# Performance work log

Measured on AMD Instinct MI355X. Metric: run time of the kernel, lower is better.

## Reference

```python
import jax, jax.numpy as jnp
from jax import lax
import numpy as np

B, COND_C = 16, 256
IN_C, OUT_C, K = 64, 64, 3
H = W = 128
N_PARAM = K * K * IN_C * OUT_C + OUT_C  # 36928


def setup_inputs() -> dict:
    key = jax.random.key(0)
    k1, k2, k3, k4 = jax.random.split(key, 4)
    x = jax.random.normal(k1, (B, IN_C, H, W), dtype=jnp.float32)
    conditioning = jax.random.normal(k2, (B, COND_C), dtype=jnp.float32)
    # nn.Linear(cond_c, n_param): weight [n_param, cond_c], bias [n_param]
    W_cond = jax.random.normal(k3, (N_PARAM, COND_C), dtype=jnp.float32) * 0.02
    b_cond = jax.random.normal(k4, (N_PARAM,), dtype=jnp.float32) * 0.02
    return {"x": x, "conditioning": conditioning, "W_cond": W_cond, "b_cond": b_cond}


def reference(x, conditioning, W_cond, b_cond):
    # Hypernetwork: Linear + tanh*5 (ConditionerActivation)
    w_b = jnp.tanh(conditioning @ W_cond.T + b_cond) * 5.0  # [B, N_PARAM]
    bias = w_b[:, -OUT_C:]                                   # [B, out_c]
    w = w_b[:, :-OUT_C].reshape(B, OUT_C, IN_C, K, K)        # per-sample OIHW

    def conv_one(xi, wi, bi):
        # xi: [in_c, H, W], wi: [out_c, in_c, K, K], bi: [out_c]
        y = lax.conv_general_dilated(
            xi[None], wi,
            window_strides=(1, 1),
            padding=[(1, 1), (1, 1)],
            dimension_numbers=("NCHW", "OIHW", "NCHW"),
        )[0]
        return y + bi[:, None, None]

    return jax.vmap(conv_one)(x, w, bias)  # [B, out_c, H, W]
```

## Files before the change

### kernel.cpp

```cpp
#include <hip/hip_runtime.h>
#include <math.h>
#include <stdint.h>

#define B_    16
#define CONDC 256
#define ICn   64
#define OCn   64
#define Hn    128
#define Wn    128
#define NW    36864
#define NPARAM 36928

typedef _Float16 half8 __attribute__((ext_vector_type(8)));
typedef _Float16 half4 __attribute__((ext_vector_type(4)));
typedef float f32x4 __attribute__((ext_vector_type(4)));
typedef float f32x16 __attribute__((ext_vector_type(16)));

__global__ __launch_bounds__(256) void prep(const float* __restrict__ x,
                                            const float* __restrict__ cond,
                                            const float* __restrict__ Wc,
                                            const float* __restrict__ bc,
                                            _Float16* __restrict__ xt,
                                            _Float16* __restrict__ wt,
                                            float* __restrict__ bias) {
    __shared__ float smem[8256];
    const int tid = threadIdx.x;
    int bx = blockIdx.x;

    if (bx < 2080) {
        const int b  = bx / 130;
        const int yp = bx - b * 130;
        _Float16* rowhalf = xt + (size_t)(b * 130 + yp) * (130 * 64);
        if (yp == 0 || yp == 129) {
            half4 z = (half4){0, 0, 0, 0};
            for (int u = tid; u < 2080; u += 256) *(half4*)(rowhalf + u * 4) = z;
            return;
        }
        float* ls = smem;
        for (int i = tid; i < 2048; i += 256) {
            int ic = i >> 5;
            float4 v = ((const float4*)x)[(((size_t)(b * 64 + ic) * 128) + (yp - 1)) * 32 + (i & 31)];
            int xx = (i & 31) * 4;
            float* lr = ls + ic * 129 + xx;
            lr[0] = v.x; lr[1] = v.y; lr[2] = v.z; lr[3] = v.w;
        }
        __syncthreads();
        for (int u2 = tid; u2 < 2080; u2 += 256) {
            int xp = u2 >> 4, ic4 = (u2 & 15) << 2;
            half4 pk;
            if (xp == 0 || xp == 129) pk = (half4){0, 0, 0, 0};
            else {
                pk[0] = (_Float16)ls[(ic4    ) * 129 + xp - 1];
                pk[1] = (_Float16)ls[(ic4 + 1) * 129 + xp - 1];
                pk[2] = (_Float16)ls[(ic4 + 2) * 129 + xp - 1];
                pk[3] = (_Float16)ls[(ic4 + 3) * 129 + xp - 1];
            }
            *(half4*)(rowhalf + u2 * 4) = pk;
        }
    } else {
        const int g = bx - 2080;
        _Float16* cl = (_Float16*)smem;
        for (int i = tid; i < 1024; i += 256) {
            float4 v = ((const float4*)cond)[i];
            half4 pk = { (_Float16)v.x, (_Float16)v.y, (_Float16)v.z, (_Float16)v.w };
            *(half4*)(cl + i * 4) = pk;
        }
        __syncthreads();
        const int w = tid >> 6, l = tid & 63;
        const int n = l & 15, r4 = l >> 4;
        const int pb = g * 64 + w * 16;

        half8 bfr[8];
        #pragma unroll
        for (int kk = 0; kk < 8; ++kk)
            bfr[kk] = *(const half8*)(cl + n * 256 + kk * 32 + r4 * 8);

        f32x4 acc = (f32x4){0.f, 0.f, 0.f, 0.f};
        const float* wr = Wc + (size_t)(pb + n) * 256 + r4 * 8;
        #pragma unroll
        for (int kk = 0; kk < 8; ++kk) {
            float4 u0 = *(const float4*)(wr + kk * 32);
            float4 u1 = *(const float4*)(wr + kk * 32 + 4);
            half8 av;
            av[0] = (_Float16)u0.x; av[1] = (_Float16)u0.y; av[2] = (_Float16)u0.z; av[3] = (_Float16)u0.w;
            av[4] = (_Float16)u1.x; av[5] = (_Float16)u1.y; av[6] = (_Float16)u1.z; av[7] = (_Float16)u1.w;
            acc = __builtin_amdgcn_mfma_f32_16x16x32_f16(av, bfr[kk], acc, 0, 0, 0);
        }
        #pragma unroll
        for (int j = 0; j < 4; ++j) {
            int p = pb + r4 * 4 + j;
            float v = tanhf(acc[j] + bc[p]) * 5.0f;
            if (p < NW) {
                int oc = p / 576, rem = p - oc * 576;
                int ic = rem / 9,  t  = rem - ic * 9;
                int icq = ic >> 4, icl = ic & 15;
                wt[((((size_t)n * 4 + icq) * 9 + t) * 64 + oc) * 16 + icl] = (_Float16)v;
            } else {
                bias[n * 64 + (p - NW)] = v;
            }
        }
    }
}

__global__ __launch_bounds__(512, 2) void conv_v4(const _Float16* __restrict__ xt,
                                                  const _Float16* __restrict__ wt,
                                                  const float* __restrict__ bias,
                                                  float* __restrict__ out) {
    __shared__ _Float16 xs[2][12288];
    const int tid = threadIdx.x;
    const int l   = tid & 63;
    const int w   = tid >> 6;
    const int px  = l & 31;
    const int jj  = l >> 5;
    const int ot  = w & 1;
    const int rg  = w >> 1;
    const int b   = blockIdx.z;
    const int X0  = blockIdx.x * 32;
    const int Y0g = blockIdx.y * 16;

    const _Float16* xbase = xt + ((size_t)(b * 130 + Y0g) * 130 + X0) * 64;
    const _Float16* wbat  = wt + (size_t)b * 36864 + (size_t)(ot * 32 + px) * 16 + jj * 8;

    int offkw[3];
    #pragma unroll
    for (int kw = 0; kw < 3; ++kw) {
        int c = (px + kw) * 2 + jj;
        offkw[kw] = (c ^ ((c >> 3) & 7)) * 16;
    }
    const int Lb = rg * 4;

    #define STAGEQ(ICQ, BUF) do {                                                       \
        _Pragma("unroll")                                                               \
        for (int it = 0; it < 3; ++it) {                                                \
            int d  = it * 512 + tid;                                                    \
            int dc = d < 1296 ? d : 1295;                                               \
            int row = (int)((unsigned)dc / 72u);                                        \
            int c   = dc - row * 72;                                                    \
            int cs  = c ^ ((c >> 3) & 7);                                               \
            const _Float16* src = xbase + (size_t)row * 8320 + (cs >> 1) * 64           \
                                + (ICQ) * 16 + (cs & 1) * 8;                            \
            __builtin_amdgcn_global_load_lds(                                           \
                (const __attribute__((address_space(1))) void*)src,                     \
                (__attribute__((address_space(3))) void*)((__attribute__((address_space(3))) char*)xs + (BUF) * 24576 + (it * 512 + (tid & ~63)) * 16), \
                16, 0, 0);                                                              \
        } } while (0)

    STAGEQ(0, 0);
    half8 A[2][9];
    #pragma unroll
    for (int t = 0; t < 9; ++t) A[0][t] = *(const half8*)(wbat + t * 1024);

    f32x16 acc[4];
    #pragma unroll
    for (int r = 0; r < 4; ++r) acc[r] = (f32x16){};

    #pragma unroll
    for (int icq = 0; icq < 4; ++icq) {
        const int cur = icq & 1;
        if (icq < 3) {
            STAGEQ(icq + 1, cur ^ 1);
            asm volatile("s_waitcnt vmcnt(3)" ::: "memory");
        } else {
            asm volatile("s_waitcnt vmcnt(0)" ::: "memory");
        }
        __builtin_amdgcn_sched_barrier(0);
        __builtin_amdgcn_s_barrier();
        __builtin_amdgcn_sched_barrier(0);

        if (icq < 3) {
            #pragma unroll
            for (int t = 0; t < 9; ++t)
                A[cur ^ 1][t] = *(const half8*)(wbat + ((icq + 1) * 9 + t) * 1024);
        }

        const char* bufb = (const char*)xs + cur * 24576;
        #pragma unroll
        for (int kw = 0; kw < 3; ++kw) {
            half8 Bf[6];
            #pragma unroll
            for (int iy = 0; iy < 6; ++iy)
                Bf[iy] = *(const half8*)(bufb + (Lb + iy) * 1152 + offkw[kw]);
            #pragma unroll
            for (int iy = 0; iy < 6; ++iy) {
                #pragma unroll
                for (int kh = 0; kh < 3; ++kh) {
                    const int r = iy - kh;
                    if (r >= 0 && r < 4)
                        acc[r] = __builtin_amdgcn_mfma_f32_32x32x16_f16(A[cur][kh * 3 + kw], Bf[iy], acc[r], 0, 0, 0);
                }
            }
        }
        asm volatile("s_waitcnt lgkmcnt(0)" ::: "memory");
        __builtin_amdgcn_sched_barrier(0);
        __builtin_amdgcn_s_barrier();
        __builtin_amdgcn_sched_barrier(0);
    }
    #undef STAGEQ

    const float* bb = bias + b * 64;
    #pragma unroll
    for (int r = 0; r < 4; ++r) {
        const int yo = Y0g + Lb + r;
        float* ob = out + (((size_t)(b * 64 + ot * 32)) * 128 + yo) * 128 + X0 + px;
        #pragma unroll
        for (int reg = 0; reg < 16; ++reg) {
            const int ocl = (reg & 3) + 8 * (reg >> 2) + 4 * jj;
            ob[(size_t)ocl * 16384] = acc[r][reg] + bb[ot * 32 + ocl];
        }
    }
}

__global__ __launch_bounds__(256) void cond_gemm(const float* __restrict__ cond,
                                                 const float* __restrict__ Wc,
                                                 const float* __restrict__ bc,
                                                 float* __restrict__ wb) {
    __shared__ float condl[B_][CONDC + 1];
    __shared__ float Wl[16][CONDC + 1];
    const int tid = threadIdx.x;
    const int p0 = blockIdx.x * 16;
    for (int i = tid; i < B_ * CONDC; i += 256) condl[i >> 8][i & 255] = cond[i];
    for (int i = tid; i < 16 * CONDC; i += 256) {
        int pl = i >> 8, k = i & 255;
        Wl[pl][k] = Wc[(p0 + pl) * CONDC + k];
    }
    __syncthreads();
    const int pl = tid >> 4;
    const int b  = tid & 15;
    float acc = bc[p0 + pl];
    #pragma unroll 8
    for (int k = 0; k < CONDC; ++k) acc += Wl[pl][k] * condl[b][k];
    wb[b * NPARAM + p0 + pl] = tanhf(acc) * 5.0f;
}

#define TS  32
#define OG  8
#define ICC 8
__global__ __launch_bounds__(256) void conv_kernel(const float* __restrict__ x,
                                                   const float* __restrict__ wb,
                                                   float* __restrict__ out) {
    __shared__ float fxs[ICC][TS + 2][TS + 2];
    __shared__ float ws[OG][ICC][9];
    const int tid = threadIdx.x;
    const int b   = blockIdx.z;
    const int ocg = blockIdx.y * OG;
    const int tx0 = (blockIdx.x & 3) * TS;
    const int ty0 = (blockIdx.x >> 2) * TS;
    const int px  = (tid & 15) * 2;
    const int py  = (tid >> 4) * 2;
    float acc[OG][4];
    #pragma unroll
    for (int o = 0; o < OG; ++o)
        #pragma unroll
        for (int q = 0; q < 4; ++q) acc[o][q] = 0.0f;
    const float* wbase = wb + b * NPARAM;
    for (int ic0 = 0; ic0 < ICn; ic0 += ICC) {
        for (int i = tid; i < ICC * (TS + 2) * (TS + 2); i += 256) {
            int icl = i / ((TS + 2) * (TS + 2));
            int rem = i % ((TS + 2) * (TS + 2));
            int yy = rem / (TS + 2), xx = rem % (TS + 2);
            int gy = ty0 - 1 + yy, gx = tx0 - 1 + xx;
            float v = 0.0f;
            if (gy >= 0 && gy < Hn && gx >= 0 && gx < Wn)
                v = x[((b * ICn + ic0 + icl) * Hn + gy) * Wn + gx];
            fxs[icl][yy][xx] = v;
        }
        for (int i = tid; i < OG * ICC * 9; i += 256) {
            int o = i / (ICC * 9), rem = i % (ICC * 9);
            int icl = rem / 9, k = rem % 9;
            ws[o][icl][k] = wbase[((ocg + o) * ICn + ic0 + icl) * 9 + k];
        }
        __syncthreads();
        #pragma unroll
        for (int icl = 0; icl < ICC; ++icl) {
            float xv[4][4];
            #pragma unroll
            for (int dy = 0; dy < 4; ++dy)
                #pragma unroll
                for (int dx = 0; dx < 4; ++dx) xv[dy][dx] = fxs[icl][py + dy][px + dx];
            #pragma unroll
            for (int o = 0; o < OG; ++o)
                #pragma unroll
                for (int kh = 0; kh < 3; ++kh)
                    #pragma unroll
                    for (int kw = 0; kw < 3; ++kw) {
                        float wv = ws[o][icl][kh * 3 + kw];
                        acc[o][0] += xv[kh][kw] * wv;
                        acc[o][1] += xv[kh][kw + 1] * wv;
                        acc[o][2] += xv[kh + 1][kw] * wv;
                        acc[o][3] += xv[kh + 1][kw + 1] * wv;
                    }
        }
        __syncthreads();
    }
    #pragma unroll
    for (int o = 0; o < OG; ++o) {
        float bias = wbase[NW + ocg + o];
        int oc = ocg + o;
        float* obase = out + ((size_t)(b * OCn + oc) * Hn + (ty0 + py)) * Wn + tx0 + px;
        obase[0] = acc[o][0] + bias;
        obase[1] = acc[o][1] + bias;
        obase[Wn] = acc[o][2] + bias;
        obase[Wn + 1] = acc[o][3] + bias;
    }
}

extern "C" void kernel_launch(void* const* d_in, const int* in_sizes, int n_in,
                              void* d_out, int out_size, void* d_ws, size_t ws_size,
                              hipStream_t stream) {
    const float* x    = (const float*)d_in[0];
    const float* cond = (const float*)d_in[1];
    const float* Wc   = (const float*)d_in[2];
    const float* bc   = (const float*)d_in[3];
    float* out = (float*)d_out;

    const size_t WT_BYTES = (size_t)B_ * 9 * 64 * 64 * 2;
    const size_t BIAS_OFF = WT_BYTES;
    const size_t XT_OFF   = 1183744;
    const size_t XT_BYTES = (size_t)B_ * 130 * 130 * 64 * 2 + 32768;
    const size_t NEED     = XT_OFF + XT_BYTES;

    if (ws_size >= NEED) {
        _Float16* wt   = (_Float16*)d_ws;
        float*    bias = (float*)((char*)d_ws + BIAS_OFF);
        _Float16* xt   = (_Float16*)((char*)d_ws + XT_OFF);
        prep<<<dim3(2080 + 577), 256, 0, stream>>>(x, cond, Wc, bc, xt, wt, bias);
        conv_v4<<<dim3(4, 8, 16), 512, 0, stream>>>(xt, wt, bias, out);
    } else {
        float* wbuf = (float*)d_ws;
        cond_gemm<<<dim3(NPARAM / 16), 256, 0, stream>>>(cond, Wc, bc, wbuf);
        conv_kernel<<<dim3(16, OCn / OG, B_), 256, 0, stream>>>(x, wbuf, out);
    }
}
```

Before: 70.09 us.

## Restructure prep kernel: packed-half transpose, separate pad blocks, finer hypernet GEMM blocks

The input-transpose blocks now pack channel pairs into 32-bit half2 words in shared memory and write 16-byte vectors, which halves LDS traffic and widens the global stores. Zero-padding rows move to their own dedicated blocks. The hypernetwork GEMM is split into twice as many smaller blocks of 32 params each, staging W_cond rows through padded LDS and converting cond on the fly. Only two of the four waves in each GEMM block do MFMA work, trading idle lanes for more parallelism across the chip. A launch-bounds occupancy hint is also added.

```diff
diff --git a/kernel.cpp b/kernel.cpp
--- a/kernel.cpp
+++ b/kernel.cpp
@@ -16,87 +16,106 @@
 typedef float f32x4 __attribute__((ext_vector_type(4)));
 typedef float f32x16 __attribute__((ext_vector_type(16)));
 
-__global__ __launch_bounds__(256) void prep(const float* __restrict__ x,
-                                            const float* __restrict__ cond,
-                                            const float* __restrict__ Wc,
-                                            const float* __restrict__ bc,
-                                            _Float16* __restrict__ xt,
-                                            _Float16* __restrict__ wt,
-                                            float* __restrict__ bias) {
-    __shared__ float smem[8256];
+__device__ inline unsigned pk2(float a, float b) {
+    union { _Float16 h[2]; unsigned u; } q;
+    q.h[0] = (_Float16)a; q.h[1] = (_Float16)b;
+    return q.u;
+}
+
+__global__ __launch_bounds__(256, 8) void prep(const float* __restrict__ x,
+                                               const float* __restrict__ cond,
+                                               const float* __restrict__ Wc,
+                                               const float* __restrict__ bc,
+                                               _Float16* __restrict__ xt,
+                                               _Float16* __restrict__ wt,
+                                               float* __restrict__ bias) {
+    __shared__ unsigned smem[4352];
     const int tid = threadIdx.x;
-    int bx = blockIdx.x;
-
-    if (bx < 2080) {
-        const int b  = bx / 130;
-        const int yp = bx - b * 130;
-        _Float16* rowhalf = xt + (size_t)(b * 130 + yp) * (130 * 64);
-        if (yp == 0 || yp == 129) {
-            half4 z = (half4){0, 0, 0, 0};
-            for (int u = tid; u < 2080; u += 256) *(half4*)(rowhalf + u * 4) = z;
-            return;
-        }
-        float* ls = smem;
-        for (int i = tid; i < 2048; i += 256) {
-            int ic = i >> 5;
-            float4 v = ((const float4*)x)[(((size_t)(b * 64 + ic) * 128) + (yp - 1)) * 32 + (i & 31)];
-            int xx = (i & 31) * 4;
-            float* lr = ls + ic * 129 + xx;
-            lr[0] = v.x; lr[1] = v.y; lr[2] = v.z; lr[3] = v.w;
+    const int bx  = blockIdx.x;
+
+    if (bx < 2048) {
+        const int b = bx >> 7, y = bx & 127, yp = y + 1;
+        const float* xrow = x + (size_t)b * 1048576 + (size_t)y * 128;
+        _Float16* rowhalf = xt + (size_t)(b * 130 + yp) * 8320;
+        unsigned* ls = smem;
+        #pragma unroll
+        for (int t = 0; t < 4; ++t) {
+            int u = t * 256 + tid;
+            int icp = u >> 5, xg = u & 31;
+            const float* r0 = xrow + (size_t)(2 * icp) * 16384;
+            float4 v0 = *((const float4*)r0 + xg);
+            float4 v1 = *((const float4*)(r0 + 16384) + xg);
+            unsigned* dst = ls + icp * 130 + 4 * xg;
+            uint2 w01 = make_uint2(pk2(v0.x, v1.x), pk2(v0.y, v1.y));
+            uint2 w23 = make_uint2(pk2(v0.z, v1.z), pk2(v0.w, v1.w));
+            *(uint2*)(dst)     = w01;
+            *(uint2*)(dst + 2) = w23;
         }
         __syncthreads();
-        for (int u2 = tid; u2 < 2080; u2 += 256) {
-            int xp = u2 >> 4, ic4 = (u2 & 15) << 2;
-            half4 pk;
-            if (xp == 0 || xp == 129) pk = (half4){0, 0, 0, 0};
-            else {
-                pk[0] = (_Float16)ls[(ic4    ) * 129 + xp - 1];
-                pk[1] = (_Float16)ls[(ic4 + 1) * 129 + xp - 1];
-                pk[2] = (_Float16)ls[(ic4 + 2) * 129 + xp - 1];
-                pk[3] = (_Float16)ls[(ic4 + 3) * 129 + xp - 1];
+        #pragma unroll
+        for (int t = 0; t < 5; ++t) {
+            int u = t * 256 + tid;
+            if (u < 1040) {
+                int xp = u >> 3, g = u & 7;
+                uint4 val = make_uint4(0u, 0u, 0u, 0u);
+                if (xp > 0 && xp < 129) {
+                    int xx = xp - 1;
+                    val.x = ls[(4 * g + 0) * 130 + xx];
+                    val.y = ls[(4 * g + 1) * 130 + xx];
+                    val.z = ls[(4 * g + 2) * 130 + xx];
+                    val.w = ls[(4 * g + 3) * 130 + xx];
+                }
+                *(uint4*)(rowhalf + (size_t)u * 8) = val;
             }
-            *(half4*)(rowhalf + u2 * 4) = pk;
-        }
+        }
+    } else if (bx < 2080) {
+        const int q = bx - 2048;
+        const int b = q >> 1, yp = (q & 1) ? 129 : 0;
+        _Float16* rowhalf = xt + (size_t)(b * 130 + yp) * 8320;
+        uint4 z = make_uint4(0u, 0u, 0u, 0u);
+        for (int u = tid; u < 1040; u += 256)
+            *(uint4*)(rowhalf + (size_t)u * 8) = z;
     } else {
         const int g = bx - 2080;
-        _Float16* cl = (_Float16*)smem;
-        for (int i = tid; i < 1024; i += 256) {
-            float4 v = ((const float4*)cond)[i];
-            half4 pk = { (_Float16)v.x, (_Float16)v.y, (_Float16)v.z, (_Float16)v.w };
-            *(half4*)(cl + i * 4) = pk;
+        const int pbase = g * 32;
+        _Float16* wl = (_Float16*)smem;
+        #pragma unroll
+        for (int t = 0; t < 8; ++t) {
+            int v = t * 256 + tid;
+            int pl = v >> 6, kg = v & 63;
+            float4 q4 = *((const float4*)(Wc + (size_t)(pbase + pl) * 256) + kg);
+            half4 h = { (_Float16)q4.x, (_Float16)q4.y, (_Float16)q4.z, (_Float16)q4.w };
+            *(half4*)(wl + pl * 272 + kg * 4) = h;
         }
         __syncthreads();
-        const int w = tid >> 6, l = tid & 63;
-        const int n = l & 15, r4 = l >> 4;
-        const int pb = g * 64 + w * 16;
-
-        half8 bfr[8];
-        #pragma unroll
-        for (int kk = 0; kk < 8; ++kk)
-            bfr[kk] = *(const half8*)(cl + n * 256 + kk * 32 + r4 * 8);
-
-        f32x4 acc = (f32x4){0.f, 0.f, 0.f, 0.f};
-        const float* wr = Wc + (size_t)(pb + n) * 256 + r4 * 8;
-        #pragma unroll
-        for (int kk = 0; kk < 8; ++kk) {
-            float4 u0 = *(const float4*)(wr + kk * 32);
-            float4 u1 = *(const float4*)(wr + kk * 32 + 4);
-            half8 av;
-            av[0] = (_Float16)u0.x; av[1] = (_Float16)u0.y; av[2] = (_Float16)u0.z; av[3] = (_Float16)u0.w;
-            av[4] = (_Float16)u1.x; av[5] = (_Float16)u1.y; av[6] = (_Float16)u1.z; av[7] = (_Float16)u1.w;
-            acc = __builtin_amdgcn_mfma_f32_16x16x32_f16(av, bfr[kk], acc, 0, 0, 0);
-        }
-        #pragma unroll
-        for (int j = 0; j < 4; ++j) {
-            int p = pb + r4 * 4 + j;
-            float v = tanhf(acc[j] + bc[p]) * 5.0f;
-            if (p < NW) {
-                int oc = p / 576, rem = p - oc * 576;
-                int ic = rem / 9,  t  = rem - ic * 9;
-                int icq = ic >> 4, icl = ic & 15;
-                wt[((((size_t)n * 4 + icq) * 9 + t) * 64 + oc) * 16 + icl] = (_Float16)v;
-            } else {
-                bias[n * 64 + (p - NW)] = v;
+        const int w = tid >> 6;
+        if (w < 2) {
+            const int l = tid & 63, n = l & 15, r4 = l >> 4;
+            const _Float16* arow = wl + (w * 16 + n) * 272 + r4 * 8;
+            const float*    crow = cond + n * 256 + r4 * 8;
+            f32x4 acc = (f32x4){0.f, 0.f, 0.f, 0.f};
+            #pragma unroll
+            for (int kk = 0; kk < 8; ++kk) {
+                half8 av = *(const half8*)(arow + kk * 32);
+                float4 u0 = *(const float4*)(crow + kk * 32);
+                float4 u1 = *(const float4*)(crow + kk * 32 + 4);
+                half8 bv;
+                bv[0] = (_Float16)u0.x; bv[1] = (_Float16)u0.y; bv[2] = (_Float16)u0.z; bv[3] = (_Float16)u0.w;
+                bv[4] = (_Float16)u1.x; bv[5] = (_Float16)u1.y; bv[6] = (_Float16)u1.z; bv[7] = (_Float16)u1.w;
+                acc = __builtin_amdgcn_mfma_f32_16x16x32_f16(av, bv, acc, 0, 0, 0);
+            }
+            #pragma unroll
+            for (int j = 0; j < 4; ++j) {
+                int p = pbase + w * 16 + r4 * 4 + j;
+                float v = tanhf(acc[j] + bc[p]) * 5.0f;
+                if (p < NW) {
+                    int oc = p / 576, rem = p - oc * 576;
+                    int ic = rem / 9,  t  = rem - ic * 9;
+                    int icq = ic >> 4, icl = ic & 15;
+                    wt[((((size_t)n * 4 + icq) * 9 + t) * 64 + oc) * 16 + icl] = (_Float16)v;
+                } else {
+                    bias[n * 64 + (p - NW)] = v;
+                }
             }
         }
     }
@@ -323,7 +342,7 @@
         _Float16* wt   = (_Float16*)d_ws;
         float*    bias = (float*)((char*)d_ws + BIAS_OFF);
         _Float16* xt   = (_Float16*)((char*)d_ws + XT_OFF);
-        prep<<<dim3(2080 + 577), 256, 0, stream>>>(x, cond, Wc, bc, xt, wt, bias);
+        prep<<<dim3(2048 + 32 + 1154), 256, 0, stream>>>(x, cond, Wc, bc, xt, wt, bias);
         conv_v4<<<dim3(4, 8, 16), 512, 0, stream>>>(xt, wt, bias, out);
     } else {
         float* wbuf = (float*)d_ws;
```

After: 67.79 us. 1.03x faster.
